# Optimization experiments

Measured on AMD Instinct MI355X. Metric: run time of the kernel, lower is better.

The kernel has to match this reference:

```python
import jax, jax.numpy as jnp
import numpy as np

B, L, D, H = 2, 2048, 2048, 16
Dh = D // H
THETA = 10000.0
NEG = -1e9


def _rope_tables(length, offset=0):
    # inv_freq: [Dh/2], positions: [L]
    inv_freq = 1.0 / (THETA ** (jnp.arange(0, Dh, 2, dtype=jnp.float32) / Dh))
    pos = jnp.arange(offset, offset + length, dtype=jnp.float32)
    freqs = pos[:, None] * inv_freq[None, :]           # [L, Dh/2]
    emb = jnp.concatenate([freqs, freqs], axis=-1)     # [L, Dh]
    return jnp.cos(emb), jnp.sin(emb)


def _rotate_half(t):
    t1, t2 = t[..., : Dh // 2], t[..., Dh // 2:]
    return jnp.concatenate([-t2, t1], axis=-1)


def setup_inputs() -> dict:
    key = jax.random.key(0)
    k1, k2, k3 = jax.random.split(key, 3)
    x = jax.random.normal(k1, (B, L, D), dtype=jnp.float32)
    attention_mask = jnp.ones((B, L), dtype=jnp.int32)
    w_qkv = jax.random.normal(k2, (D, 3 * D), dtype=jnp.float32) * (D ** -0.5)
    w_proj = jax.random.normal(k3, (D, D), dtype=jnp.float32) * (D ** -0.5)
    return {"x": x, "attention_mask": attention_mask, "w_qkv": w_qkv, "w_proj": w_proj}


def reference(x, attention_mask, w_qkv, w_proj):
    # QKV projection (no bias)
    qkv = x @ w_qkv                                    # [B, L, 3D]
    q, k, v = jnp.split(qkv, 3, axis=-1)
    q = q.reshape(B, L, H, Dh).transpose(0, 2, 1, 3)   # [B, H, L, Dh]
    k = k.reshape(B, L, H, Dh).transpose(0, 2, 1, 3)
    v = v.reshape(B, L, H, Dh).transpose(0, 2, 1, 3)

    # RoPE (past_len = 0)
    cos, sin = _rope_tables(L)                         # [L, Dh]
    q = q * cos + _rotate_half(q) * sin
    k = k * cos + _rotate_half(k) * sin

    # causal + key-padding mask (True = masked out)
    causal = jnp.triu(jnp.ones((L, L), dtype=bool), k=1)         # [L, L]
    pad = (attention_mask == 0)[:, None, None, :]                # [B,1,1,L]
    mask = causal[None, None, :, :] | pad                        # [B,1,L,L]

    scale = Dh ** -0.5
    scores = jnp.einsum("bhqd,bhkd->bhqk", q, k) * scale         # [B,H,L,L]
    scores = jnp.where(mask, NEG, scores)
    attn = jax.nn.softmax(scores, axis=-1)
    y = jnp.einsum("bhqk,bhkd->bhqd", attn, v)                   # [B,H,L,Dh]
    y = y.transpose(0, 2, 1, 3).reshape(B, L, D)
    return y @ w_proj
```

## Files before the change

### kernel.cpp

```cpp
#include <hip/hip_runtime.h>
#include <hip/hip_bf16.h>

typedef unsigned short ushort_t;
typedef __attribute__((ext_vector_type(4))) float fvec4;
typedef __attribute__((ext_vector_type(16))) float fvec16;
typedef __attribute__((ext_vector_type(8))) short short8;
typedef __attribute__((ext_vector_type(4))) unsigned short usvec4;
typedef __attribute__((ext_vector_type(2))) unsigned int uvec2;

typedef const __attribute__((address_space(1))) void* gas_ptr;
typedef __attribute__((address_space(3))) void* las_ptr;

__device__ __forceinline__ void glds16(const void* g, void* l) {
  __builtin_amdgcn_global_load_lds((gas_ptr)g, (las_ptr)l, 16, 0, 0);
}

__device__ __forceinline__ ushort_t f2bf(float f) {
  unsigned u = __float_as_uint(f);
  u += 0x7FFFu + ((u >> 16) & 1u);
  return (ushort_t)(u >> 16);
}
__device__ __forceinline__ float bf2f(ushort_t h) {
  return __uint_as_float(((unsigned)h) << 16);
}

__device__ __forceinline__ void swap32(unsigned& a, unsigned& b) {
#if __has_builtin(__builtin_amdgcn_permlane32_swap)
  uvec2 r = __builtin_amdgcn_permlane32_swap(a, b, false, false);
  a = r[0]; b = r[1];
#else
  const unsigned sa = (unsigned)__shfl_xor((int)a, 32);
  const unsigned sb = (unsigned)__shfl_xor((int)b, 32);
  const bool hi = (threadIdx.x & 32) != 0;
  const unsigned na = hi ? sb : a;
  const unsigned nb = hi ? b : sa;
  a = na; b = nb;
#endif
}

__global__ __launch_bounds__(256) void cast_f32_bf16(const float* __restrict__ X,
                                                     ushort_t* __restrict__ Xb) {
  const size_t i = ((size_t)blockIdx.x * 256 + threadIdx.x) * 4;
  const fvec4 v = *(const fvec4*)(X + i);
  usvec4 o;
  o[0] = f2bf(v[0]); o[1] = f2bf(v[1]); o[2] = f2bf(v[2]); o[3] = f2bf(v[3]);
  *(usvec4*)(Xb + i) = o;
}

__global__ __launch_bounds__(256) void tcast(const float* __restrict__ W,
                                             ushort_t* __restrict__ Wt,
                                             const int Kd, const int Nd) {
  __shared__ float ls[64][65];
  const int t = threadIdx.x;
  const int n0 = blockIdx.x * 64, k0 = blockIdx.y * 64;
  const int kr = t >> 4, nc = (t & 15) * 4;
#pragma unroll
  for (int it = 0; it < 4; ++it) {
    const fvec4 v = *(const fvec4*)(W + (size_t)(k0 + it * 16 + kr) * Nd + n0 + nc);
    ls[it * 16 + kr][nc + 0] = v[0];
    ls[it * 16 + kr][nc + 1] = v[1];
    ls[it * 16 + kr][nc + 2] = v[2];
    ls[it * 16 + kr][nc + 3] = v[3];
  }
  __syncthreads();
  const int nr = t >> 2, kg = (t & 3) * 16;
  __align__(16) ushort_t tmp[16];
#pragma unroll
  for (int i = 0; i < 16; ++i) tmp[i] = f2bf(ls[kg + i][nr]);
  ushort_t* dst = Wt + (size_t)(n0 + nr) * Kd + k0 + kg;
  *(short8*)(dst)     = *(const short8*)(tmp);
  *(short8*)(dst + 8) = *(const short8*)(tmp + 8);
}

#define FENCE asm volatile("" ::: "memory")

__device__ __forceinline__ void stage_one(const ushort_t* __restrict__ G, const int grow,
                                          const int K, const int tk, ushort_t* ldsmat,
                                          const int lrow0, const int wv, const int lane) {
  const int rr = lane >> 3;
  const int kk = ((lane & 7) ^ rr) * 8;
  glds16(G + (size_t)(grow + wv * 8 + rr) * K + tk + kk,
         ldsmat + (lrow0 + wv * 8) * 64);
}

__device__ __forceinline__ short8 frag_ld(const ushort_t* ldsmat, const int rbase,
                                          const int kc, const int quad, const int mm) {
  const int r = rbase + mm;
  const int blk = r >> 6;
  const int pblk = ((blk & 1) << 1) | (blk >> 1);
  const int ldsrow = pblk * 64 + (r & 63);
  const int kb = (kc * 64 + quad * 16) ^ ((mm & 7) << 4);
  return *(const short8*)(ldsmat + ldsrow * 64 + (kb >> 1));
}

__device__ __forceinline__ short8 fragld128(const ushort_t* mat, const int row,
                                            const int kc, const int quad) {
  const int kb = (kc * 64 + quad * 16) ^ ((row & 7) << 4);
  return *(const short8*)(mat + row * 64 + (kb >> 1));
}

#define G192_RD_A(dst_, Am, q_)                                               \
  dst_[0][0] = frag_ld(Am, wr * 128 + (q_) * 32,      0, quad, mm);           \
  dst_[0][1] = frag_ld(Am, wr * 128 + (q_) * 32,      1, quad, mm);           \
  dst_[1][0] = frag_ld(Am, wr * 128 + (q_) * 32 + 16, 0, quad, mm);           \
  dst_[1][1] = frag_ld(Am, wr * 128 + (q_) * 32 + 16, 1, quad, mm);

#define G192_RD_B(dst_, Bm)                                                   \
  _Pragma("unroll")                                                           \
  for (int j = 0; j < 3; ++j) {                                               \
    dst_[j][0] = fragld128(Bm, wc * 48 + j * 16 + mm, 0, quad);               \
    dst_[j][1] = fragld128(Bm, wc * 48 + j * 16 + mm, 1, quad);               \
  }

#define G192_MFMA(af_, bf_, q_)                                               \
  __builtin_amdgcn_s_setprio(1);                                              \
  _Pragma("unroll")                                                           \
  for (int ii = 0; ii < 2; ++ii)                                              \
  _Pragma("unroll")                                                           \
  for (int j = 0; j < 3; ++j) {                                               \
    acc[(q_) * 2 + ii][j] = __builtin_amdgcn_mfma_f32_16x16x32_bf16(          \
        af_[ii][0], bf_[j][0], acc[(q_) * 2 + ii][j], 0, 0, 0);               \
    acc[(q_) * 2 + ii][j] = __builtin_amdgcn_mfma_f32_16x16x32_bf16(          \
        af_[ii][1], bf_[j][1], acc[(q_) * 2 + ii][j], 0, 0, 0);               \
  }                                                                           \
  __builtin_amdgcn_s_setprio(0);                                              \
  __builtin_amdgcn_sched_barrier(0);

__global__ __launch_bounds__(512, 2) void gemm192p(
    const ushort_t* __restrict__ A, const ushort_t* __restrict__ Bt,
    const int M, const int N, const int K, const int mode,
    float* __restrict__ C,
    ushort_t* __restrict__ Qo, ushort_t* __restrict__ Ko, ushort_t* __restrict__ Vo) {
  __shared__ __align__(16) ushort_t lds[2][28672];

  const int tid = threadIdx.x, wv = tid >> 6, lane = tid & 63;
  const int quad = lane >> 4, mm = lane & 15;
  const int wr = wv >> 2, wc = wv & 3;

  const int nwg = gridDim.x, ntx = N / 192;
  const int bid = blockIdx.x;
  const int swz = (bid & 7) * (nwg >> 3) + (bid >> 3);
  const int by = swz / ntx, bx = swz - by * ntx;
  const int row0 = by * 256, col0 = bx * 192;

  fvec4 acc[8][3];
#pragma unroll
  for (int i = 0; i < 8; ++i)
#pragma unroll
    for (int j = 0; j < 3; ++j) acc[i][j] = (fvec4){0.f, 0.f, 0.f, 0.f};

  short8 bfrE[3][2], bfrO[3][2];
  short8 afE[2][2], afO[2][2];

  ushort_t* A0 = &lds[0][0];      ushort_t* B0 = &lds[0][16384];
  ushort_t* A1 = &lds[1][0];      ushort_t* B1 = &lds[1][16384];

  stage_one(Bt, col0 + 0,   K, 0,  B0, 0,   wv, lane); FENCE;
  stage_one(Bt, col0 + 64,  K, 0,  B0, 64,  wv, lane); FENCE;
  stage_one(Bt, col0 + 128, K, 0,  B0, 128, wv, lane); FENCE;
  stage_one(A,  row0 + 0,   K, 0,  A0, 0,   wv, lane); FENCE;
  stage_one(A,  row0 + 64,  K, 0,  A0, 128, wv, lane); FENCE;
  stage_one(A,  row0 + 128, K, 0,  A0, 64,  wv, lane); FENCE;
  stage_one(A,  row0 + 192, K, 0,  A0, 192, wv, lane); FENCE;
  stage_one(Bt, col0 + 0,   K, 64, B1, 0,   wv, lane); FENCE;
  stage_one(Bt, col0 + 64,  K, 64, B1, 64,  wv, lane); FENCE;
  stage_one(Bt, col0 + 128, K, 64, B1, 128, wv, lane); FENCE;
  stage_one(A,  row0 + 0,   K, 64, A1, 0,   wv, lane); FENCE;
  stage_one(A,  row0 + 128, K, 64, A1, 64,  wv, lane); FENCE;
  asm volatile("s_waitcnt vmcnt(5)" ::: "memory");
  __builtin_amdgcn_s_barrier();
  G192_RD_B(bfrE, B0);
  G192_RD_A(afE, A0, 0);

  const int nit = K >> 7;
  for (int i = 0; i < nit; ++i) {
    const bool more = (i + 1 < nit);
    const int kA = i * 128 + 64;
    const int kB = i * 128 + 128;
    const int kC = i * 128 + 192;
    {
      __builtin_amdgcn_s_barrier();
      stage_one(A, row0 + 64,  K, kA, A1, 128, wv, lane); FENCE;
      stage_one(A, row0 + 192, K, kA, A1, 192, wv, lane);
      G192_MFMA(afE, bfrE, 0);
      G192_RD_A(afO, A0, 1);
    }
    {
      __builtin_amdgcn_s_barrier();
      if (more) { stage_one(Bt, col0 + 0,  K, kB, B0, 0,  wv, lane); FENCE;
                  stage_one(Bt, col0 + 64, K, kB, B0, 64, wv, lane); }
      G192_MFMA(afO, bfrE, 1);
      G192_RD_A(afE, A0, 2);
    }
    {
      __builtin_amdgcn_s_barrier();
      if (more) { stage_one(Bt, col0 + 128, K, kB, B0, 128, wv, lane);
                  asm volatile("s_waitcnt vmcnt(3)" ::: "memory");
      } else {    asm volatile("s_waitcnt vmcnt(0)" ::: "memory"); }
      G192_MFMA(afE, bfrE, 2);
      G192_RD_A(afO, A0, 3);
    }
    {
      __builtin_amdgcn_s_barrier();
      if (more) { stage_one(A, row0 + 0,   K, kB, A0, 0,  wv, lane); FENCE;
                  stage_one(A, row0 + 128, K, kB, A0, 64, wv, lane); }
      G192_MFMA(afO, bfrE, 3);
      G192_RD_B(bfrO, B1);
      G192_RD_A(afE, A1, 0);
    }
    {
      __builtin_amdgcn_s_barrier();
      if (more) { stage_one(A, row0 + 64,  K, kB, A0, 128, wv, lane); FENCE;
                  stage_one(A, row0 + 192, K, kB, A0, 192, wv, lane); }
      G192_MFMA(afE, bfrO, 0);
      G192_RD_A(afO, A1, 1);
    }
    {
      __builtin_amdgcn_s_barrier();
      if (more) { stage_one(Bt, col0 + 0,  K, kC, B1, 0,  wv, lane); FENCE;
                  stage_one(Bt, col0 + 64, K, kC, B1, 64, wv, lane); }
      G192_MFMA(afO, bfrO, 1);
      G192_RD_A(afE, A1, 2);
    }
    {
      __builtin_amdgcn_s_barrier();
      if (more) { stage_one(Bt, col0 + 128, K, kC, B1, 128, wv, lane);
                  asm volatile("s_waitcnt vmcnt(3)" ::: "memory"); }
      G192_MFMA(afE, bfrO, 2);
      G192_RD_A(afO, A1, 3);
    }
    {
      __builtin_amdgcn_s_barrier();
      if (more) { stage_one(A, row0 + 0,   K, kC, A1, 0,  wv, lane); FENCE;
                  stage_one(A, row0 + 128, K, kC, A1, 64, wv, lane); }
      G192_MFMA(afO, bfrO, 3);
      if (more) { G192_RD_B(bfrE, B0); G192_RD_A(afE, A0, 0); }
    }
  }

  if (mode == 0) {
#pragma unroll
    for (int i = 0; i < 8; ++i)
#pragma unroll
      for (int r = 0; r < 4; ++r) {
        const int row = row0 + wr * 128 + i * 16 + quad * 4 + r;
        float* cr = C + (size_t)row * N + col0 + wc * 48;
#pragma unroll
        for (int j = 0; j < 3; ++j) cr[j * 16 + mm] = acc[i][j][r];
      }
  } else {
#pragma unroll
    for (int j = 0; j < 3; ++j) {
      const int gcolj = col0 + wc * 48 + j * 16;
      const int which = gcolj >> 11;
      const int h = (gcolj >> 7) & 15;
      const int coff = (gcolj & 127) + mm;
      ushort_t* dst = (which == 0) ? Qo : (which == 1) ? Ko : Vo;
#pragma unroll
      for (int i = 0; i < 8; ++i)
#pragma unroll
        for (int r = 0; r < 4; ++r) {
          const int row = row0 + wr * 128 + i * 16 + quad * 4 + r;
          const int bb = row >> 11, l = row & 2047;
          dst[((size_t)(bb * 16 + h) * 2048 + l) * 128 + coff] = f2bf(acc[i][j][r]);
        }
    }
  }
}

__device__ __forceinline__ void stage_a128(const ushort_t* __restrict__ G, const int row0,
                                           const int K, const int tk, ushort_t* ldsA,
                                           const int wv, const int lane) {
  const int rr = lane >> 3;
  const int kk = ((lane & 7) ^ rr) * 8;
  const int r = wv * 8 + rr;
  glds16(G + (size_t)(row0 + r) * K + tk + kk,      ldsA + (wv * 8) * 64);
  glds16(G + (size_t)(row0 + 64 + r) * K + tk + kk, ldsA + (64 + wv * 8) * 64);
}
__device__ __forceinline__ void stage_b128(const ushort_t* __restrict__ G, const int col0,
                                           const int K, const int tk, ushort_t* ldsB,
                                           const int u, const int wv, const int lane) {
  const int rr = lane >> 3;
  const int kk = ((lane & 7) ^ rr) * 8;
  const int r = u * 64 + wv * 8 + rr;
  glds16(G + (size_t)(col0 + r) * K + tk + kk,       ldsB + (u * 64 + wv * 8) * 64);
  glds16(G + (size_t)(col0 + 128 + r) * K + tk + kk, ldsB + (128 + u * 64 + wv * 8) * 64);
}

__global__ __launch_bounds__(512, 2) void gemm128(
    const ushort_t* __restrict__ A, const ushort_t* __restrict__ Bt,
    const int M, const int N, const int K, const int mode,
    float* __restrict__ C,
    ushort_t* __restrict__ Qo, ushort_t* __restrict__ Ko, ushort_t* __restrict__ Vo) {
  __shared__ __align__(16) ushort_t l128[2][24576];

  const int tid = threadIdx.x, wv = tid >> 6, lane = tid & 63;
  const int quad = lane >> 4, mm = lane & 15;
  const int wr = wv >> 2, wc = wv & 3;

  const int nwg = gridDim.x, ntx = N >> 8;
  const int bid = blockIdx.x;
  const int swz = (bid & 7) * (nwg >> 3) + (bid >> 3);
  const int by = swz / ntx, bx = swz - by * ntx;
  const int row0 = by * 128, col0 = bx * 256;

  fvec4 acc[4][4];
#pragma unroll
  for (int m = 0; m < 4; ++m)
#pragma unroll
    for (int j = 0; j < 4; ++j) acc[m][j] = (fvec4){0.f, 0.f, 0.f, 0.f};

  ushort_t* A0 = &l128[0][0];     ushort_t* B0 = &l128[0][8192];
  ushort_t* A1 = &l128[1][0];     ushort_t* B1 = &l128[1][8192];

  short8 bfr[4][2];

  stage_b128(Bt, col0, K, 0,  B0, 0, wv, lane); FENCE;
  stage_b128(Bt, col0, K, 0,  B0, 1, wv, lane); FENCE;
  stage_a128(A,  row0, K, 0,  A0,    wv, lane); FENCE;
  stage_b128(Bt, col0, K, 64, B1, 0, wv, lane); FENCE;
  stage_b128(Bt, col0, K, 64, B1, 1, wv, lane); FENCE;
  asm volatile("s_waitcnt vmcnt(4)" ::: "memory");
  __builtin_amdgcn_s_barrier();

  const int nit = K >> 7;
  for (int i = 0; i < nit; ++i) {
    const bool more = (i + 1 < nit);
    const int kA = i * 128 + 64;
    const int kB = i * 128 + 128;
    const int kC = i * 128 + 192;
    {
      stage_a128(A, row0, K, kA, A1, wv, lane);
      short8 af[4];
#pragma unroll
      for (int m = 0; m < 4; ++m) af[m] = fragld128(A0, wr * 64 + m * 16 + mm, 0, quad);
#pragma unroll
      for (int j = 0; j < 4; ++j) {
        bfr[j][0] = fragld128(B0, wc * 64 + j * 16 + mm, 0, quad);
        bfr[j][1] = fragld128(B0, wc * 64 + j * 16 + mm, 1, quad);
      }
      __builtin_amdgcn_s_setprio(1);
#pragma unroll
      for (int m = 0; m < 4; ++m)
#pragma unroll
        for (int j = 0; j < 4; ++j)
          acc[m][j] = __builtin_amdgcn_mfma_f32_16x16x32_bf16(af[m], bfr[j][0], acc[m][j], 0, 0, 0);
      __builtin_amdgcn_s_setprio(0);
      asm volatile("s_waitcnt lgkmcnt(0)" ::: "memory");
      __builtin_amdgcn_sched_barrier(0);
    }
    {
      __builtin_amdgcn_s_barrier();
      if (more) { stage_b128(Bt, col0, K, kB, B0, 0, wv, lane); FENCE;
                  stage_b128(Bt, col0, K, kB, B0, 1, wv, lane); FENCE; }
      if (more) { asm volatile("s_waitcnt vmcnt(4)" ::: "memory"); }
      else      { asm volatile("s_waitcnt vmcnt(0)" ::: "memory"); }
      short8 af[4];
#pragma unroll
      for (int m = 0; m < 4; ++m) af[m] = fragld128(A0, wr * 64 + m * 16 + mm, 1, quad);
      __builtin_amdgcn_s_setprio(1);
#pragma unroll
      for (int m = 0; m < 4; ++m)
#pragma unroll
        for (int j = 0; j < 4; ++j)
          acc[m][j] = __builtin_amdgcn_mfma_f32_16x16x32_bf16(af[m], bfr[j][1], acc[m][j], 0, 0, 0);
      __builtin_amdgcn_s_setprio(0);
    }
    {
      __builtin_amdgcn_s_barrier();
      if (more) stage_a128(A, row0, K, kB, A0, wv, lane);
      short8 af[4];
#pragma unroll
      for (int m = 0; m < 4; ++m) af[m] = fragld128(A1, wr * 64 + m * 16 + mm, 0, quad);
#pragma unroll
      for (int j = 0; j < 4; ++j) {
        bfr[j][0] = fragld128(B1, wc * 64 + j * 16 + mm, 0, quad);
        bfr[j][1] = fragld128(B1, wc * 64 + j * 16 + mm, 1, quad);
      }
      __builtin_amdgcn_s_setprio(1);
#pragma unroll
      for (int m = 0; m < 4; ++m)
#pragma unroll
        for (int j = 0; j < 4; ++j)
          acc[m][j] = __builtin_amdgcn_mfma_f32_16x16x32_bf16(af[m], bfr[j][0], acc[m][j], 0, 0, 0);
      __builtin_amdgcn_s_setprio(0);
      asm volatile("s_waitcnt lgkmcnt(0)" ::: "memory");
      __builtin_amdgcn_sched_barrier(0);
    }
    {
      __builtin_amdgcn_s_barrier();
      if (more) { stage_b128(Bt, col0, K, kC, B1, 0, wv, lane); FENCE;
                  stage_b128(Bt, col0, K, kC, B1, 1, wv, lane); FENCE;
                  asm volatile("s_waitcnt vmcnt(4)" ::: "memory"); }
      short8 af[4];
#pragma unroll
      for (int m = 0; m < 4; ++m) af[m] = fragld128(A1, wr * 64 + m * 16 + mm, 1, quad);
      __builtin_amdgcn_s_setprio(1);
#pragma unroll
      for (int m = 0; m < 4; ++m)
#pragma unroll
        for (int j = 0; j < 4; ++j)
          acc[m][j] = __builtin_amdgcn_mfma_f32_16x16x32_bf16(af[m], bfr[j][1], acc[m][j], 0, 0, 0);
      __builtin_amdgcn_s_setprio(0);
      __builtin_amdgcn_s_barrier();
    }
  }

  if (mode == 0) {
#pragma unroll
    for (int m = 0; m < 4; ++m)
#pragma unroll
      for (int r = 0; r < 4; ++r) {
        const int row = row0 + wr * 64 + m * 16 + quad * 4 + r;
        float* cr = C + (size_t)row * N + col0 + wc * 64;
#pragma unroll
        for (int j = 0; j < 4; ++j) cr[j * 16 + mm] = acc[m][j][r];
      }
  } else {
    const int gcol = col0 + wc * 64;
    const int which = gcol >> 11;
    const int h = (gcol >> 7) & 15;
    const int coff = gcol & 127;
    ushort_t* dst = (which == 0) ? Qo : (which == 1) ? Ko : Vo;
#pragma unroll
    for (int m = 0; m < 4; ++m)
#pragma unroll
      for (int r = 0; r < 4; ++r) {
        const int row = row0 + wr * 64 + m * 16 + quad * 4 + r;
        const int bb = row >> 11, l = row & 2047;
        ushort_t* dr = dst + ((size_t)(bb * 16 + h) * 2048 + l) * 128 + coff;
#pragma unroll
        for (int j = 0; j < 4; ++j) dr[j * 16 + mm] = f2bf(acc[m][j][r]);
      }
  }
}

__global__ __launch_bounds__(256) void rope_kernel(ushort_t* Qb, ushort_t* Kb) {
  const int gid = blockIdx.x * 256 + threadIdx.x;
  const int pd0 = (gid & 7) * 8;
  const int row = gid >> 3;
  const int l = row & 2047;
  ushort_t* base = (blockIdx.y ? Kb : Qb) + (size_t)row * 128;
  const short8 va = *(const short8*)(base + pd0);
  const short8 vb = *(const short8*)(base + pd0 + 64);
  short8 oa, ob;
  const float fl = (float)l;
  const bool isQ = (blockIdx.y == 0);
#pragma unroll
  for (int i = 0; i < 8; ++i) {
    const int pd = pd0 + i;
    const float a  = bf2f((ushort_t)va[i]);
    const float bv = bf2f((ushort_t)vb[i]);
    const float invf_rev = exp2f(-(float)pd * 0.20762050593045702f) * 0.15915494309189535f;
    float rev = fl * invf_rev;
    rev -= floorf(rev);
    const float ang = rev * 6.283185307179586f;
    float s, c;
    __sincosf(ang, &s, &c);
    float na = a * c - bv * s;
    float nb = bv * c + a * s;
    if (isQ) { na *= 0.08838834764831845f; nb *= 0.08838834764831845f; }
    oa[i] = (short)f2bf(na);
    ob[i] = (short)f2bf(nb);
  }
  *(short8*)(base + pd0)      = oa;
  *(short8*)(base + pd0 + 64) = ob;
}

__global__ __launch_bounds__(256) void vtrans_kernel(const ushort_t* __restrict__ Vn,
                                                     ushort_t* __restrict__ Vt) {
  __shared__ ushort_t ls[128 * 132];
  const int bh = blockIdx.x >> 4;
  const int l0 = (blockIdx.x & 15) * 128;
  const int t = threadIdx.x;
  const ushort_t* src = Vn + ((size_t)bh * 2048 + l0) * 128;
#pragma unroll
  for (int it = 0; it < 16; ++it) {
    const int c = it * 256 + t;
    const int lr = c >> 5, dc = (c & 31) * 4;
    *(usvec4*)(ls + lr * 132 + dc) = *(const usvec4*)(src + lr * 128 + dc);
  }
  __syncthreads();
  ushort_t* dstb = Vt + (size_t)bh * 128 * 2048 + l0;
#pragma unroll
  for (int it = 0; it < 16; ++it) {
    const int c = it * 256 + t;
    const int d = c >> 5, lc = (c & 31) * 4;
    usvec4 o;
    o[0] = ls[(lc + 0) * 132 + d];
    o[1] = ls[(lc + 1) * 132 + d];
    o[2] = ls[(lc + 2) * 132 + d];
    o[3] = ls[(lc + 3) * 132 + d];
    *(usvec4*)(dstb + (size_t)d * 2048 + lc) = o;
  }
}

__global__ __launch_bounds__(256, 2) void flash_kernel(
    const ushort_t* __restrict__ Qb, const ushort_t* __restrict__ Kb,
    const ushort_t* __restrict__ Vt, const int* __restrict__ am,
    ushort_t* __restrict__ Y) {
  __shared__ __align__(16) ushort_t lK[2][8192];
  __shared__ __align__(16) ushort_t lV[2][8192];
  __shared__ float lds_l[128];

  const int tid = threadIdx.x, wv = tid >> 6, lane = tid & 63;
  const int lh = lane >> 5, cq = lane & 31;
  const int bid = blockIdx.x;
  const int bh = bid & 31;
  const int idx = (bid >> 5) & 7;
  const int qi = (bid >> 8) ? (15 - idx) : idx;
  const int b = bh >> 4, head = bh & 15;
  const size_t qkBase = (size_t)bh * (2048 * 128);
  const int qb = qi * 128 + wv * 32;
  const int q = qb + cq;

  unsigned fullbits = 0;
  {
    const int* amr = am + b * 2048;
#pragma unroll
    for (int rgn = 0; rgn < 4; ++rgn) {
      const int4 a0 = *(const int4*)(amr + rgn * 512 + lane * 8);
      const int4 a1 = *(const int4*)(amr + rgn * 512 + lane * 8 + 4);
      const bool ok8 = a0.x && a0.y && a0.z && a0.w && a1.x && a1.y && a1.z && a1.w;
      const unsigned long long bal = __ballot(ok8);
#pragma unroll
      for (int tt = 0; tt < 8; ++tt)
        fullbits |= ((((bal >> (8 * tt)) & 0xFFull) == 0xFFull) ? 1u : 0u) << (rgn * 8 + tt);
    }
  }

  short8 qf[8];
  {
    const ushort_t* qrow = Qb + qkBase + (size_t)q * 128;
#pragma unroll
    for (int c = 0; c < 8; ++c) qf[c] = *(const short8*)(qrow + c * 16 + lh * 8);
  }

  fvec16 yacc[4];
#pragma unroll
  for (int i = 0; i < 4; ++i)
#pragma unroll
    for (int r = 0; r < 16; ++r) yacc[i][r] = 0.f;
  float psum = 0.f;

#define FLASH_STAGE(dK, dV, kk0)                                                          \
  _Pragma("unroll")                                                                       \
  for (int it = 0; it < 4; ++it) {                                                        \
    const int f_ = it * 4 + wv;                                                           \
    const int ct_ = f_ >> 3, c_ = f_ & 7;                                                 \
    glds16(Kb + qkBase + (size_t)((kk0) + ct_ * 32 + cq) * 128 + c_ * 16 + lh * 8,        \
           (dK) + f_ * 512);                                                              \
    const int dt_ = f_ >> 2, kc_ = f_ & 3;                                                \
    glds16(Vt + ((size_t)bh * 128 + dt_ * 32 + cq) * 2048 + (kk0) + kc_ * 16 + lh * 8,    \
           (dV) + f_ * 512);                                                              \
  }

  const int nt = qi * 2 + 2;
  FLASH_STAGE(&lK[0][0], &lV[0][0], 0)
  __syncthreads();

  int cur = 0;
  for (int t = 0; t < nt; ++t) {
    const int k0 = t * 64;
    if (t + 1 < nt) {
      FLASH_STAGE(&lK[cur ^ 1][0], &lV[cur ^ 1][0], k0 + 64)
    }

    if (k0 <= qb + 31) {
      const ushort_t* bK = &lK[cur][0];
      const ushort_t* bV = &lV[cur][0];
      const bool maskfull = (fullbits >> t) & 1u;
      unsigned long long keymask = ~0ull;
      if (!maskfull) keymask = __ballot(am[b * 2048 + k0 + lane] != 0);
      const bool fullvalid = (k0 + 63 <= qb) && maskfull;

#pragma unroll
      for (int ct = 0; ct < 2; ++ct) {
        fvec16 sA_, sB_;
#pragma unroll
        for (int r = 0; r < 16; ++r) { sA_[r] = 0.f; sB_[r] = 0.f; }
        __builtin_amdgcn_s_setprio(1);
#pragma unroll
        for (int c = 0; c < 4; ++c) {
          short8 kf = *(const short8*)(bK + (ct * 8 + c) * 512 + lane * 8);
          sA_ = __builtin_amdgcn_mfma_f32_32x32x16_bf16(kf, qf[c], sA_, 0, 0, 0);
        }
#pragma unroll
        for (int c = 4; c < 8; ++c) {
          short8 kf = *(const short8*)(bK + (ct * 8 + c) * 512 + lane * 8);
          sB_ = __builtin_amdgcn_mfma_f32_32x32x16_bf16(kf, qf[c], sB_, 0, 0, 0);
        }
        __builtin_amdgcn_s_setprio(0);
        float p[16];
        if (fullvalid) {
#pragma unroll
          for (int r = 0; r < 16; ++r) p[r] = __expf(sA_[r] + sB_[r]);
        } else {
#pragma unroll
          for (int r = 0; r < 16; ++r) {
            const int kl = (r & 3) + 8 * (r >> 2) + 4 * lh + ct * 32;
            const bool ok = (k0 + kl <= q) && (((keymask >> kl) & 1ull) != 0);
            p[r] = ok ? __expf(sA_[r] + sB_[r]) : 0.f;
          }
        }
#pragma unroll
        for (int r = 0; r < 16; ++r) psum += p[r];
        unsigned pk[8];
#pragma unroll
        for (int j = 0; j < 8; ++j) {
          __hip_bfloat162 t2 = __float22bfloat162_rn(make_float2(p[2 * j], p[2 * j + 1]));
          pk[j] = *(unsigned*)&t2;
        }
#pragma unroll
        for (int kc2 = 0; kc2 < 2; ++kc2) {
          unsigned a0 = pk[kc2 * 4 + 0], a2 = pk[kc2 * 4 + 2];
          unsigned a1 = pk[kc2 * 4 + 1], a3 = pk[kc2 * 4 + 3];
          swap32(a0, a2);
          swap32(a1, a3);
          union { unsigned u[4]; short8 s; } pf;
          pf.u[0] = a0; pf.u[1] = a1; pf.u[2] = a2; pf.u[3] = a3;
          const int kc = ct * 2 + kc2;
          __builtin_amdgcn_s_setprio(1);
#pragma unroll
          for (int dt = 0; dt < 4; ++dt) {
            short8 vf = *(const short8*)(bV + (dt * 4 + kc) * 512 + lane * 8);
            yacc[dt] = __builtin_amdgcn_mfma_f32_32x32x16_bf16(pf.s, vf, yacc[dt], 0, 0, 0);
          }
          __builtin_amdgcn_s_setprio(0);
        }
      }
    }
    __syncthreads();
    cur ^= 1;
  }
#undef FLASH_STAGE

  psum += __shfl_xor(psum, 32);
  if (lane < 32) lds_l[wv * 32 + lane] = psum;
  float inv16[16];
#pragma unroll
  for (int r = 0; r < 16; ++r)
    inv16[r] = 1.f / lds_l[wv * 32 + (r & 3) + 8 * (r >> 2) + 4 * lh];

#pragma unroll
  for (int dt = 0; dt < 4; ++dt)
#pragma unroll
    for (int r = 0; r < 16; ++r) {
      const int qloc = (r & 3) + 8 * (r >> 2) + 4 * lh;
      ushort_t* dst = Y + ((size_t)(b * 2048 + qb + qloc)) * 2048 + head * 128 + dt * 32 + cq;
      *dst = f2bf(yacc[dt][r] * inv16[r]);
    }
}

extern "C" void kernel_launch(void* const* d_in, const int* in_sizes, int n_in,
                              void* d_out, int out_size, void* d_ws, size_t ws_size,
                              hipStream_t stream) {
  const float* x      = (const float*)d_in[0];
  const int*   amask  = (const int*)d_in[1];
  const float* w_qkv  = (const float*)d_in[2];
  const float* w_proj = (const float*)d_in[3];

  ushort_t* xb     = (ushort_t*)d_ws;
  ushort_t* wqkvT  = xb + 8388608;
  ushort_t* wprojT = wqkvT + 12582912;
  ushort_t* Qb     = wprojT + 4194304;
  ushort_t* Kb     = Qb + 8388608;
  ushort_t* Vn     = Kb + 8388608;
  ushort_t* Vt     = wqkvT;
  ushort_t* Yb     = xb;

  cast_f32_bf16<<<8192, 256, 0, stream>>>(x, xb);
  tcast<<<dim3(96, 32), 256, 0, stream>>>(w_qkv, wqkvT, 2048, 6144);
  tcast<<<dim3(32, 32), 256, 0, stream>>>(w_proj, wprojT, 2048, 2048);
  gemm192p<<<512, 512, 0, stream>>>(xb, wqkvT, 4096, 6144, 2048, 1,
                                    nullptr, Qb, Kb, Vn);
  rope_kernel<<<dim3(2048, 2), 256, 0, stream>>>(Qb, Kb);
  vtrans_kernel<<<512, 256, 0, stream>>>(Vn, Vt);
  flash_kernel<<<512, 256, 0, stream>>>(Qb, Kb, Vt, amask, Yb);
  gemm128<<<256, 512, 0, stream>>>(Yb, wprojT, 4096, 2048, 2048, 0,
                                   (float*)d_out, nullptr, nullptr, nullptr);
}
```

Before: 388.6 us.

## Fuse V transpose into QKV GEMM epilogue, Q RoPE into flash, merge weight casts

The QKV GEMM epilogue now writes V directly in transposed [bh][d][l] layout with 4-wide vector stores, which removes the separate vtrans kernel and its full read/write pass over V. Q RoPE and the softmax scale are applied in registers inside the flash kernel after Q is loaded, so the RoPE kernel only processes K. The two weight transpose-cast launches are merged into one launch. This saves several launches and memory passes, at the cost of strided V stores in the GEMM epilogue and extra per-block sincos work in the flash kernel.

```diff
diff --git a/kernel.cpp b/kernel.cpp
--- a/kernel.cpp
+++ b/kernel.cpp
@@ -47,12 +47,18 @@
   *(usvec4*)(Xb + i) = o;
 }
 
-__global__ __launch_bounds__(256) void tcast(const float* __restrict__ W,
-                                             ushort_t* __restrict__ Wt,
-                                             const int Kd, const int Nd) {
+__global__ __launch_bounds__(256) void tcast2(const float* __restrict__ Wq,
+                                              ushort_t* __restrict__ Wqt,
+                                              const float* __restrict__ Wp,
+                                              ushort_t* __restrict__ Wpt) {
   __shared__ float ls[64][65];
   const int t = threadIdx.x;
-  const int n0 = blockIdx.x * 64, k0 = blockIdx.y * 64;
+  int bx = blockIdx.x;
+  const float* W; ushort_t* Wt; int Nd;
+  if (bx < 96) { W = Wq; Wt = Wqt; Nd = 6144; }
+  else         { bx -= 96; W = Wp; Wt = Wpt; Nd = 2048; }
+  const int Kd = 2048;
+  const int n0 = bx * 64, k0 = blockIdx.y * 64;
   const int kr = t >> 4, nc = (t & 15) * 4;
 #pragma unroll
   for (int it = 0; it < 4; ++it) {
@@ -255,15 +261,27 @@
       const int which = gcolj >> 11;
       const int h = (gcolj >> 7) & 15;
       const int coff = (gcolj & 127) + mm;
-      ushort_t* dst = (which == 0) ? Qo : (which == 1) ? Ko : Vo;
-#pragma unroll
-      for (int i = 0; i < 8; ++i)
-#pragma unroll
-        for (int r = 0; r < 4; ++r) {
-          const int row = row0 + wr * 128 + i * 16 + quad * 4 + r;
+      if (which == 2) {
+#pragma unroll
+        for (int i = 0; i < 8; ++i) {
+          const int row = row0 + wr * 128 + i * 16 + quad * 4;
           const int bb = row >> 11, l = row & 2047;
-          dst[((size_t)(bb * 16 + h) * 2048 + l) * 128 + coff] = f2bf(acc[i][j][r]);
+          usvec4 o;
+#pragma unroll
+          for (int r = 0; r < 4; ++r) o[r] = f2bf(acc[i][j][r]);
+          *(usvec4*)(Vo + ((size_t)(bb * 16 + h) * 128 + coff) * 2048 + l) = o;
         }
+      } else {
+        ushort_t* dst = (which == 0) ? Qo : Ko;
+#pragma unroll
+        for (int i = 0; i < 8; ++i)
+#pragma unroll
+          for (int r = 0; r < 4; ++r) {
+            const int row = row0 + wr * 128 + i * 16 + quad * 4 + r;
+            const int bb = row >> 11, l = row & 2047;
+            dst[((size_t)(bb * 16 + h) * 2048 + l) * 128 + coff] = f2bf(acc[i][j][r]);
+          }
+      }
     }
   }
 }
@@ -435,17 +453,16 @@
   }
 }
 
-__global__ __launch_bounds__(256) void rope_kernel(ushort_t* Qb, ushort_t* Kb) {
+__global__ __launch_bounds__(256) void ropek_kernel(ushort_t* Kb) {
   const int gid = blockIdx.x * 256 + threadIdx.x;
   const int pd0 = (gid & 7) * 8;
   const int row = gid >> 3;
   const int l = row & 2047;
-  ushort_t* base = (blockIdx.y ? Kb : Qb) + (size_t)row * 128;
+  ushort_t* base = Kb + (size_t)row * 128;
   const short8 va = *(const short8*)(base + pd0);
   const short8 vb = *(const short8*)(base + pd0 + 64);
   short8 oa, ob;
   const float fl = (float)l;
-  const bool isQ = (blockIdx.y == 0);
 #pragma unroll
   for (int i = 0; i < 8; ++i) {
     const int pd = pd0 + i;
@@ -457,42 +474,11 @@
     const float ang = rev * 6.283185307179586f;
     float s, c;
     __sincosf(ang, &s, &c);
-    float na = a * c - bv * s;
-    float nb = bv * c + a * s;
-    if (isQ) { na *= 0.08838834764831845f; nb *= 0.08838834764831845f; }
-    oa[i] = (short)f2bf(na);
-    ob[i] = (short)f2bf(nb);
+    oa[i] = (short)f2bf(a * c - bv * s);
+    ob[i] = (short)f2bf(bv * c + a * s);
   }
   *(short8*)(base + pd0)      = oa;
   *(short8*)(base + pd0 + 64) = ob;
-}
-
-__global__ __launch_bounds__(256) void vtrans_kernel(const ushort_t* __restrict__ Vn,
-                                                     ushort_t* __restrict__ Vt) {
-  __shared__ ushort_t ls[128 * 132];
-  const int bh = blockIdx.x >> 4;
-  const int l0 = (blockIdx.x & 15) * 128;
-  const int t = threadIdx.x;
-  const ushort_t* src = Vn + ((size_t)bh * 2048 + l0) * 128;
-#pragma unroll
-  for (int it = 0; it < 16; ++it) {
-    const int c = it * 256 + t;
-    const int lr = c >> 5, dc = (c & 31) * 4;
-    *(usvec4*)(ls + lr * 132 + dc) = *(const usvec4*)(src + lr * 128 + dc);
-  }
-  __syncthreads();
-  ushort_t* dstb = Vt + (size_t)bh * 128 * 2048 + l0;
-#pragma unroll
-  for (int it = 0; it < 16; ++it) {
-    const int c = it * 256 + t;
-    const int d = c >> 5, lc = (c & 31) * 4;
-    usvec4 o;
-    o[0] = ls[(lc + 0) * 132 + d];
-    o[1] = ls[(lc + 1) * 132 + d];
-    o[2] = ls[(lc + 2) * 132 + d];
-    o[3] = ls[(lc + 3) * 132 + d];
-    *(usvec4*)(dstb + (size_t)d * 2048 + lc) = o;
-  }
 }
 
 __global__ __launch_bounds__(256, 2) void flash_kernel(
@@ -534,6 +520,23 @@
     const ushort_t* qrow = Qb + qkBase + (size_t)q * 128;
 #pragma unroll
     for (int c = 0; c < 8; ++c) qf[c] = *(const short8*)(qrow + c * 16 + lh * 8);
+    const float fl = (float)q;
+#pragma unroll
+    for (int c = 0; c < 4; ++c)
+#pragma unroll
+      for (int j = 0; j < 8; ++j) {
+        const int pd = c * 16 + lh * 8 + j;
+        const float a  = bf2f((ushort_t)qf[c][j]);
+        const float bv = bf2f((ushort_t)qf[c + 4][j]);
+        const float invf_rev = exp2f(-(float)pd * 0.20762050593045702f) * 0.15915494309189535f;
+        float rev = fl * invf_rev;
+        rev -= floorf(rev);
+        const float ang = rev * 6.283185307179586f;
+        float s, cs;
+        __sincosf(ang, &s, &cs);
+        qf[c][j]     = (short)f2bf((a * cs - bv * s) * 0.08838834764831845f);
+        qf[c + 4][j] = (short)f2bf((bv * cs + a * s) * 0.08838834764831845f);
+      }
   }
 
   fvec16 yacc[4];
@@ -665,17 +668,14 @@
   ushort_t* wprojT = wqkvT + 12582912;
   ushort_t* Qb     = wprojT + 4194304;
   ushort_t* Kb     = Qb + 8388608;
-  ushort_t* Vn     = Kb + 8388608;
-  ushort_t* Vt     = wqkvT;
+  ushort_t* Vt     = Kb + 8388608;
   ushort_t* Yb     = xb;
 
   cast_f32_bf16<<<8192, 256, 0, stream>>>(x, xb);
-  tcast<<<dim3(96, 32), 256, 0, stream>>>(w_qkv, wqkvT, 2048, 6144);
-  tcast<<<dim3(32, 32), 256, 0, stream>>>(w_proj, wprojT, 2048, 2048);
+  tcast2<<<dim3(128, 32), 256, 0, stream>>>(w_qkv, wqkvT, w_proj, wprojT);
   gemm192p<<<512, 512, 0, stream>>>(xb, wqkvT, 4096, 6144, 2048, 1,
-                                    nullptr, Qb, Kb, Vn);
-  rope_kernel<<<dim3(2048, 2), 256, 0, stream>>>(Qb, Kb);
-  vtrans_kernel<<<512, 256, 0, stream>>>(Vn, Vt);
+                                    nullptr, Qb, Kb, Vt);
+  ropek_kernel<<<2048, 256, 0, stream>>>(Kb);
   flash_kernel<<<512, 256, 0, stream>>>(Qb, Kb, Vt, amask, Yb);
   gemm128<<<256, 512, 0, stream>>>(Yb, wprojT, 4096, 2048, 2048, 0,
                                    (float*)d_out, nullptr, nullptr, nullptr);
```

New measurement: 360.0 us. 7.4% less time.
